# Kernel optimization log

Measured on AMD Instinct MI355X. Metric: run time of the kernel, lower is better.

Reference implementation:

```python
import jax, jax.numpy as jnp
import numpy as np

N = 16384      # nodes
E = 131072     # edges
D = 768        # in_size = hid_size = out_size (LayerNorm(768) hardcoded)
NT = 4         # num edge types (TypedLinear num_types)
NB = 3         # num bases (basis regularizer)
LN_EPS = 1e-5


def _layernorm(x, gamma, beta):
    mu = jnp.mean(x, axis=-1, keepdims=True)
    var = jnp.mean(jnp.square(x - mu), axis=-1, keepdims=True)
    return (x - mu) * jax.lax.rsqrt(var + LN_EPS) * gamma + beta


def setup_inputs() -> dict:
    key = jax.random.key(0)
    ks = jax.random.split(key, 16)
    s = 0.02  # weight init scale
    return {
        "h": jax.random.normal(ks[0], (N, D), jnp.float32),
        # TypedLinear basis params: W = sum_b coeff[t,b] * basis[b]
        "W_text": jax.random.normal(ks[1], (NB, D, D), jnp.float32) * s,
        "coeff_text": jax.random.normal(ks[2], (NT, NB), jnp.float32),
        "W_user": jax.random.normal(ks[3], (NB, D, D), jnp.float32) * s,
        "coeff_user": jax.random.normal(ks[4], (NT, NB), jnp.float32),
        "W_dst": jax.random.normal(ks[5], (NB, D, D), jnp.float32) * s,
        "coeff_dst": jax.random.normal(ks[6], (NT, NB), jnp.float32),
        "ln_gamma": jnp.ones((D,), jnp.float32),
        "ln_beta": jnp.zeros((D,), jnp.float32),
        "W_lin": jax.random.normal(ks[7], (2 * D, D), jnp.float32) * s,
        "b_lin": jnp.zeros((D,), jnp.float32),
        "src": jax.random.randint(ks[8], (E,), 0, N, dtype=jnp.int32),
        "dst": jax.random.randint(ks[9], (E,), 0, N, dtype=jnp.int32),
        "etype": jax.random.randint(ks[10], (E,), 0, NT, dtype=jnp.int32),
        "hete": jax.random.randint(ks[11], (E,), 0, 2, dtype=jnp.int32),
    }


def reference(h, W_text, coeff_text, W_user, coeff_user, W_dst, coeff_dst,
              ln_gamma, ln_beta, W_lin, b_lin, src, dst, etype, hete):
    # eval mode: dropout = identity
    x = _layernorm(h, ln_gamma, ln_beta)                       # [N, D]
    # Typed-linear via basis decomposition, folded per (type, node): [NT, N, D]
    Ht = jnp.einsum('nd,bdh,tb->tnh', x, W_text, coeff_text)
    Hu = jnp.einsum('nd,bdh,tb->tnh', x, W_user, coeff_user)
    Hd = jnp.einsum('nd,bdh,tb->tnh', x, W_dst, coeff_dst)

    mask = hete > 0                                            # hete vs homo edges
    # per-edge routed source message: [E, D]
    ef = jnp.where(mask[:, None],
                   jax.nn.relu(Ht[etype, src]),
                   jax.nn.relu(Hu[etype, src]))
    # Original concatenates [hete_feat, homo_feat] along edge dim, i.e. a stable
    # permutation putting hete edges first; dst features stay in original order.
    perm = jnp.argsort((~mask).astype(jnp.int32), stable=True)
    feat_perm = ef[perm]                                       # [E, D]
    dfeat = jax.nn.relu(Hd[etype, dst])                        # [E, D]
    m = jnp.concatenate([feat_perm, dfeat], axis=-1)           # [E, 2D]
    # scatter-sum messages to destination nodes
    n = jax.ops.segment_sum(m, dst, num_segments=N)            # [N, 2D]
    z = jax.nn.relu(n @ W_lin + b_lin)                         # [N, D]
    zn = jnp.linalg.norm(z, ord=2, axis=1, keepdims=True)
    zn = jnp.where(zn == 0, jnp.asarray(1.0, z.dtype), zn)
    return z / zn
```

## Files before the change

kernel.cpp:

```cpp
#include <hip/hip_runtime.h>
#include <hip/hip_bf16.h>
#include <cstdint>

static constexpr int N_  = 16384;
static constexpr int E_  = 131072;
static constexpr int D_  = 768;
static constexpr int D2_ = 1536;
static constexpr int DSQ_ = D_ * D_;

static constexpr size_t OFF_XB   = 0;
static constexpr size_t OFF_WCT  = 25165824;
static constexpr size_t OFF_WLT  = 39321600;
static constexpr size_t OFF_NB16 = 41680896;
static constexpr size_t OFF_H4   = 92012544;
static constexpr size_t OFF_ZB   = 92012544;
static constexpr size_t OFF_N1C  = 192675840;
static constexpr size_t OFF_TG   = 217841664;
static constexpr size_t OFF_PAY  = 218365952;
static constexpr size_t OFF_CNT  = 218890240;
static constexpr size_t OFF_BASE = 219152384;
static constexpr size_t OFF_CUR  = 219217936;
static constexpr size_t OFF_BC   = 219283472;
static constexpr size_t OFF_SCAN = 219285520;

typedef __attribute__((ext_vector_type(8))) short short8v;
typedef __attribute__((ext_vector_type(4))) float floatx4;

__device__ __forceinline__ void gld16(const void* g, void* l) {
  __builtin_amdgcn_global_load_lds(
      (const __attribute__((address_space(1))) unsigned int*)g,
      (__attribute__((address_space(3))) unsigned int*)l, 16, 0, 0);
}

__device__ __forceinline__ float b2f(short u) {
  union { unsigned int i; float f; } x;
  x.i = ((unsigned int)(unsigned short)u) << 16;
  return x.f;
}

__device__ __forceinline__ float wave_sum(float v) {
#pragma unroll
  for (int o = 32; o; o >>= 1) v += __shfl_down(v, o, 64);
  return v;
}

__global__ __launch_bounds__(256) void combine_wt_kernel(
    const float* __restrict__ Wt, const float* __restrict__ ct,
    const float* __restrict__ Wu, const float* __restrict__ cu,
    const float* __restrict__ Wd, const float* __restrict__ cd,
    __hip_bfloat16* __restrict__ WcT) {
  int i  = blockIdx.x * 256 + threadIdx.x;
  int ft = blockIdx.y;
  int f = ft >> 2, t = ft & 3;
  const float* W = (f == 0) ? Wt : ((f == 1) ? Wu : Wd);
  const float* c = ((f == 0) ? ct : ((f == 1) ? cu : cd)) + t * 3;
  float v = c[0] * W[i] + c[1] * W[DSQ_ + i] + c[2] * W[2 * DSQ_ + i];
  int d = i / D_, h = i % D_;
  WcT[(size_t)ft * DSQ_ + (size_t)h * D_ + d] = __float2bfloat16(v);
}

__global__ __launch_bounds__(256) void wlint_kernel(
    const float* __restrict__ W, __hip_bfloat16* __restrict__ WT) {
  int i = blockIdx.x * 256 + threadIdx.x;
  int k = i / D_, h = i % D_;
  WT[(size_t)h * D2_ + k] = __float2bfloat16(W[i]);
}

__global__ __launch_bounds__(256) void ln_kernel(
    const float* __restrict__ h, const float* __restrict__ gamma,
    const float* __restrict__ beta, __hip_bfloat16* __restrict__ x) {
  int v = blockIdx.x, tid = threadIdx.x;
  const float* hr = h + (size_t)v * D_;
  float e0 = hr[tid], e1 = hr[tid + 256], e2 = hr[tid + 512];
  float s = e0 + e1 + e2;
  float q = e0 * e0 + e1 * e1 + e2 * e2;
  __shared__ float red[8];
  __shared__ float mv[2];
  float ws_ = wave_sum(s), wq = wave_sum(q);
  int lane = tid & 63, w = tid >> 6;
  if (lane == 0) { red[w] = ws_; red[4 + w] = wq; }
  __syncthreads();
  if (tid == 0) {
    float S = red[0] + red[1] + red[2] + red[3];
    float Q = red[4] + red[5] + red[6] + red[7];
    float mu = S * (1.0f / D_);
    float var = Q * (1.0f / D_) - mu * mu;
    mv[0] = mu;
    mv[1] = rsqrtf(var + 1e-5f);
  }
  __syncthreads();
  float mu = mv[0], rstd = mv[1];
  __hip_bfloat16* xr = x + (size_t)v * D_;
  xr[tid]       = __float2bfloat16((e0 - mu) * rstd * gamma[tid]       + beta[tid]);
  xr[tid + 256] = __float2bfloat16((e1 - mu) * rstd * gamma[tid + 256] + beta[tid + 256]);
  xr[tid + 512] = __float2bfloat16((e2 - mu) * rstd * gamma[tid + 512] + beta[tid + 512]);
}

__global__ __launch_bounds__(256) void edge_a_kernel(
    const int* __restrict__ hete, const int* __restrict__ dst,
    const int* __restrict__ etype, int* __restrict__ blockcnt,
    int* __restrict__ cnt4) {
  int j = blockIdx.x * 256 + threadIdx.x;
  int flag = hete[j] > 0;
  unsigned long long m = __ballot(flag);
  __shared__ int wsum[4];
  int lane = threadIdx.x & 63, w = threadIdx.x >> 6;
  if (lane == 0) wsum[w] = __popcll(m);
  __syncthreads();
  if (threadIdx.x == 0)
    blockcnt[blockIdx.x] = wsum[0] + wsum[1] + wsum[2] + wsum[3];
  atomicAdd(&cnt4[dst[j] * 4 + etype[j]], 1);
}

__global__ __launch_bounds__(512) void scan_kernel(
    const int* __restrict__ blockcnt, int* __restrict__ scanout) {
  __shared__ int s[512];
  int t = threadIdx.x;
  int v = blockcnt[t];
  s[t] = v;
  __syncthreads();
  for (int o = 1; o < 512; o <<= 1) {
    int add = (t >= o) ? s[t - o] : 0;
    __syncthreads();
    s[t] += add;
    __syncthreads();
  }
  scanout[t] = s[t] - v;
  if (t == 511) scanout[512] = s[511];
}

__global__ __launch_bounds__(256) void edge_b_kernel(
    const int* __restrict__ hete, const int* __restrict__ dst,
    const int* __restrict__ scanout, int* __restrict__ target) {
  int j = blockIdx.x * 256 + threadIdx.x;
  int flag = hete[j] > 0;
  unsigned long long m = __ballot(flag);
  __shared__ int wsum[4];
  int lane = threadIdx.x & 63, w = threadIdx.x >> 6;
  if (lane == 0) wsum[w] = __popcll(m);
  __syncthreads();
  int wpre = 0;
#pragma unroll
  for (int i = 0; i < 4; i++) wpre += (i < w) ? wsum[i] : 0;
  int lpre = __popcll(m & ((1ull << lane) - 1ull));
  int hcum = scanout[blockIdx.x] + wpre + lpre;
  int K = scanout[512];
  int e = flag ? hcum : (K + j - hcum);
  target[j] = dst[e];
}

__global__ __launch_bounds__(1024) void base_scan_kernel(
    const int* __restrict__ cnt4, int* __restrict__ base) {
  __shared__ int s[1024];
  int t = threadIdx.x;
  int loc[16];
  int sum = 0;
#pragma unroll
  for (int i = 0; i < 16; i++) {
    int v = t * 16 + i;
    int d = cnt4[v * 4] + cnt4[v * 4 + 1] + cnt4[v * 4 + 2] + cnt4[v * 4 + 3];
    loc[i] = sum;
    sum += d;
  }
  s[t] = sum;
  __syncthreads();
  for (int o = 1; o < 1024; o <<= 1) {
    int add = (t >= o) ? s[t - o] : 0;
    __syncthreads();
    s[t] += add;
    __syncthreads();
  }
  int pre = t ? s[t - 1] : 0;
#pragma unroll
  for (int i = 0; i < 16; i++) base[t * 16 + i] = pre + loc[i];
  if (t == 1023) base[N_] = s[1023];
}

__global__ __launch_bounds__(256) void edge_sort_kernel(
    const int* __restrict__ target, const int* __restrict__ src,
    const int* __restrict__ etype, const int* __restrict__ hete,
    const int* __restrict__ base, int* __restrict__ cursor,
    int* __restrict__ payload) {
  int j = blockIdx.x * 256 + threadIdx.x;
  int v = target[j];
  int p = base[v] + atomicAdd(&cursor[v], 1);
  int g = ((hete[j] > 0) ? 0 : 4) + etype[j];
  payload[p] = (g << 14) | src[j];
}

template <bool FIRST>
__global__ __launch_bounds__(256) void gather_n1_kernel(
    const __hip_bfloat16* __restrict__ H, const int* __restrict__ base,
    const int* __restrict__ payload, __hip_bfloat16* __restrict__ n1c,
    __hip_bfloat16* __restrict__ nb16, int g0) {
  int wv = threadIdx.x >> 6, lane = threadIdx.x & 63;
  int v = blockIdx.x * 4 + wv;
  int b0 = base[v], b1 = base[v + 1];
  float acc[12];
  if (FIRST) {
#pragma unroll
    for (int i = 0; i < 12; i++) acc[i] = 0.f;
  } else {
    short8v a8 = *(const short8v*)(n1c + (size_t)v * D_ + lane * 8);
    short4  b4 = *(const short4*)(n1c + (size_t)v * D_ + 512 + lane * 4);
#pragma unroll
    for (int i = 0; i < 8; i++) acc[i] = b2f(a8[i]);
    acc[8] = b2f(b4.x); acc[9] = b2f(b4.y);
    acc[10] = b2f(b4.z); acc[11] = b2f(b4.w);
  }
  for (int idx = b0; idx < b1; ++idx) {
    int pl = payload[idx];
    int g = (pl >> 14) - g0;
    if ((unsigned)g > 3u) continue;
    const __hip_bfloat16* row = H + ((size_t)g * N_ + (pl & 16383)) * D_;
    short8v a8 = *(const short8v*)(row + lane * 8);
    short4  b4 = *(const short4*)(row + 512 + lane * 4);
#pragma unroll
    for (int i = 0; i < 8; i++) acc[i] += b2f(a8[i]);
    acc[8] += b2f(b4.x); acc[9] += b2f(b4.y);
    acc[10] += b2f(b4.z); acc[11] += b2f(b4.w);
  }
  __hip_bfloat16 o[12];
#pragma unroll
  for (int i = 0; i < 12; i++) o[i] = __float2bfloat16(acc[i]);
  if (FIRST) {
    *(short8v*)(n1c + (size_t)v * D_ + lane * 8) = *(const short8v*)o;
    *(short4*)(n1c + (size_t)v * D_ + 512 + lane * 4) = *(const short4*)(o + 8);
  } else {
    *(short8v*)(nb16 + (size_t)v * D2_ + lane * 8) = *(const short8v*)o;
    *(short4*)(nb16 + (size_t)v * D2_ + 512 + lane * 4) = *(const short4*)(o + 8);
  }
}

__global__ __launch_bounds__(256) void combine_n2_kernel(
    const __hip_bfloat16* __restrict__ H4, const int* __restrict__ cnt4,
    __hip_bfloat16* __restrict__ nb16) {
  size_t i = ((size_t)blockIdx.x * 256 + threadIdx.x) * 8;
  int v = (int)(i / D_);
  int k = (int)(i % D_);
  float acc[8] = {0.f, 0.f, 0.f, 0.f, 0.f, 0.f, 0.f, 0.f};
#pragma unroll
  for (int t = 0; t < 4; t++) {
    float c = (float)cnt4[v * 4 + t];
    if (c != 0.f) {
      short8v hv = *(const short8v*)(H4 + (size_t)t * N_ * D_ + i);
#pragma unroll
      for (int j = 0; j < 8; j++) acc[j] += c * b2f(hv[j]);
    }
  }
  __hip_bfloat16 o[8];
#pragma unroll
  for (int j = 0; j < 8; j++) o[j] = __float2bfloat16(acc[j]);
  *(short8v*)(nb16 + (size_t)v * D2_ + D_ + k) = *(const short8v*)o;
}

template <bool BIAS, bool OUTBF16>
__global__ __launch_bounds__(256) void gemm_mfma_kernel(
    const __hip_bfloat16* __restrict__ A, const __hip_bfloat16* __restrict__ BT0,
    const float* __restrict__ bias, void* __restrict__ Cv,
    int M, int N, int K, size_t strideB, size_t strideC) {
  const __hip_bfloat16* BT = BT0 + (size_t)blockIdx.z * strideB;
  __shared__ char lds[32768];
  char* As = lds;
  char* Bs = lds + 16384;
  int tid = threadIdx.x;
  int lane = tid & 63;
  int wv = tid >> 6;
  int wr = wv >> 1, wc = wv & 1;
  int nwg = gridDim.x * gridDim.y;
  int id = blockIdx.y * gridDim.x + blockIdx.x;
  int s = (id & 7) * (nwg >> 3) + (id >> 3);
  int bx = s % gridDim.x, by = s / gridDim.x;
  int row0 = by * 128, col0 = bx * 128;
  int r_ = tid >> 3;
  int s_ = tid & 7;

  floatx4 acc[4][4];
#pragma unroll
  for (int i = 0; i < 4; i++)
#pragma unroll
    for (int j = 0; j < 4; j++) acc[i][j] = floatx4{0.f, 0.f, 0.f, 0.f};

  for (int k0 = 0; k0 < K; k0 += 64) {
    __syncthreads();
#pragma unroll
    for (int is = 0; is < 4; is++) {
      int r = is * 32 + r_;
      int sp = s_ ^ (r & 7);
      gld16(A  + (size_t)(row0 + r) * K + k0 + sp * 8, As + is * 4096 + tid * 16);
      gld16(BT + (size_t)(col0 + r) * K + k0 + sp * 8, Bs + is * 4096 + tid * 16);
    }
    __syncthreads();
#pragma unroll
    for (int kk = 0; kk < 64; kk += 32) {
      int p = (kk >> 3) + (lane >> 4);
      short8v af[4], bf[4];
#pragma unroll
      for (int m = 0; m < 4; m++) {
        int ra = wr * 64 + m * 16 + (lane & 15);
        af[m] = *(const short8v*)(As + ra * 128 + ((p ^ (ra & 7)) << 4));
        int rb = wc * 64 + m * 16 + (lane & 15);
        bf[m] = *(const short8v*)(Bs + rb * 128 + ((p ^ (rb & 7)) << 4));
      }
#pragma unroll
      for (int m = 0; m < 4; m++)
#pragma unroll
        for (int n = 0; n < 4; n++)
          acc[m][n] = __builtin_amdgcn_mfma_f32_16x16x32_bf16(
              af[m], bf[n], acc[m][n], 0, 0, 0);
    }
  }
#pragma unroll
  for (int m = 0; m < 4; m++) {
#pragma unroll
    for (int n = 0; n < 4; n++) {
      int col = col0 + wc * 64 + n * 16 + (lane & 15);
      float bv = BIAS ? bias[col] : 0.f;
#pragma unroll
      for (int q = 0; q < 4; q++) {
        int row = row0 + wr * 64 + m * 16 + (lane >> 4) * 4 + q;
        float v = fmaxf(acc[m][n][q] + bv, 0.f);
        if constexpr (OUTBF16) {
          ((__hip_bfloat16*)Cv + (size_t)blockIdx.z * strideC)
              [(size_t)row * N + col] = __float2bfloat16(v);
        } else {
          ((float*)Cv + (size_t)blockIdx.z * strideC)
              [(size_t)row * N + col] = v;
        }
      }
    }
  }
}

__global__ __launch_bounds__(256) void norm_kernel(
    const float* __restrict__ z, float* __restrict__ out) {
  int v = blockIdx.x, tid = threadIdx.x;
  const float* zr = z + (size_t)v * D_;
  float e0 = zr[tid], e1 = zr[tid + 256], e2 = zr[tid + 512];
  float q = e0 * e0 + e1 * e1 + e2 * e2;
  __shared__ float red[4];
  __shared__ float sc;
  float wq = wave_sum(q);
  int lane = tid & 63, w = tid >> 6;
  if (lane == 0) red[w] = wq;
  __syncthreads();
  if (tid == 0) {
    float S = red[0] + red[1] + red[2] + red[3];
    float norm = sqrtf(S);
    sc = (norm == 0.f) ? 1.f : (1.f / norm);
  }
  __syncthreads();
  float s = sc;
  float* orow = out + (size_t)v * D_;
  orow[tid]       = e0 * s;
  orow[tid + 256] = e1 * s;
  orow[tid + 512] = e2 * s;
}

extern "C" void kernel_launch(void* const* d_in, const int* in_sizes, int n_in,
                              void* d_out, int out_size, void* d_ws,
                              size_t ws_size, hipStream_t stream) {
  (void)in_sizes; (void)n_in; (void)out_size; (void)ws_size;
  const float* h      = (const float*)d_in[0];
  const float* W_text = (const float*)d_in[1];
  const float* c_text = (const float*)d_in[2];
  const float* W_user = (const float*)d_in[3];
  const float* c_user = (const float*)d_in[4];
  const float* W_dst  = (const float*)d_in[5];
  const float* c_dst  = (const float*)d_in[6];
  const float* gamma  = (const float*)d_in[7];
  const float* beta   = (const float*)d_in[8];
  const float* W_lin  = (const float*)d_in[9];
  const float* b_lin  = (const float*)d_in[10];
  const int* src      = (const int*)d_in[11];
  const int* dst      = (const int*)d_in[12];
  const int* etype    = (const int*)d_in[13];
  const int* hete     = (const int*)d_in[14];
  float* out          = (float*)d_out;

  char* ws = (char*)d_ws;
  __hip_bfloat16* xb   = (__hip_bfloat16*)(ws + OFF_XB);
  __hip_bfloat16* WcT  = (__hip_bfloat16*)(ws + OFF_WCT);
  __hip_bfloat16* WlT  = (__hip_bfloat16*)(ws + OFF_WLT);
  __hip_bfloat16* nb16 = (__hip_bfloat16*)(ws + OFF_NB16);
  __hip_bfloat16* H4   = (__hip_bfloat16*)(ws + OFF_H4);
  float* zbuf          = (float*)(ws + OFF_ZB);
  __hip_bfloat16* n1c  = (__hip_bfloat16*)(ws + OFF_N1C);
  int* target   = (int*)(ws + OFF_TG);
  int* payload  = (int*)(ws + OFF_PAY);
  int* cnt4     = (int*)(ws + OFF_CNT);
  int* base     = (int*)(ws + OFF_BASE);
  int* cursor   = (int*)(ws + OFF_CUR);
  int* blockcnt = (int*)(ws + OFF_BC);
  int* scanout  = (int*)(ws + OFF_SCAN);

  hipMemsetAsync(cnt4, 0, (size_t)N_ * 4 * 4, stream);
  hipMemsetAsync(cursor, 0, (size_t)N_ * 4, stream);

  combine_wt_kernel<<<dim3(DSQ_ / 256, 12), 256, 0, stream>>>(
      W_text, c_text, W_user, c_user, W_dst, c_dst, WcT);
  wlint_kernel<<<(D2_ * D_) / 256, 256, 0, stream>>>(W_lin, WlT);
  ln_kernel<<<N_, 256, 0, stream>>>(h, gamma, beta, xb);
  edge_a_kernel<<<E_ / 256, 256, 0, stream>>>(hete, dst, etype, blockcnt, cnt4);
  scan_kernel<<<1, 512, 0, stream>>>(blockcnt, scanout);
  edge_b_kernel<<<E_ / 256, 256, 0, stream>>>(hete, dst, scanout, target);
  base_scan_kernel<<<1, 1024, 0, stream>>>(cnt4, base);
  edge_sort_kernel<<<E_ / 256, 256, 0, stream>>>(target, src, etype, hete,
                                                 base, cursor, payload);

  const size_t HSTRIDE = (size_t)N_ * D_;

  gemm_mfma_kernel<false, true>
      <<<dim3(D_ / 128, N_ / 128, 4), 256, 0, stream>>>(
          xb, WcT + (size_t)8 * DSQ_, nullptr, H4, N_, D_, D_, DSQ_, HSTRIDE);
  combine_n2_kernel<<<(N_ * D_) / (256 * 8), 256, 0, stream>>>(H4, cnt4, nb16);

  gemm_mfma_kernel<false, true>
      <<<dim3(D_ / 128, N_ / 128, 4), 256, 0, stream>>>(
          xb, WcT, nullptr, H4, N_, D_, D_, DSQ_, HSTRIDE);
  gather_n1_kernel<true><<<N_ / 4, 256, 0, stream>>>(H4, base, payload, n1c,
                                                     nb16, 0);
  gemm_mfma_kernel<false, true>
      <<<dim3(D_ / 128, N_ / 128, 4), 256, 0, stream>>>(
          xb, WcT + (size_t)4 * DSQ_, nullptr, H4, N_, D_, D_, DSQ_, HSTRIDE);
  gather_n1_kernel<false><<<N_ / 4, 256, 0, stream>>>(H4, base, payload, n1c,
                                                      nb16, 4);

  gemm_mfma_kernel<true, false>
      <<<dim3(D_ / 128, N_ / 128, 1), 256, 0, stream>>>(
          nb16, WlT, b_lin, zbuf, N_, D_, D2_, 0, 0);
  norm_kernel<<<N_, 256, 0, stream>>>(zbuf, out);
}
```

Baseline: 509.6 us.

## Replace GEMM with 256x128 tile, 512 threads, triple-buffered LDS pipeline

The bf16 MFMA GEMM is rewritten to use 256x128 output tiles with 8 waves and a three-stage LDS ring buffer. Global loads for k+2 are issued while MFMAs run on stage k, with explicit vmcnt/lgkmcnt waits, raised wave priority around the MFMAs, and two barrier phases per k-step. The intent is to hide global-load latency and raise reuse of the B tile. It uses 144KB of LDS per workgroup, which limits occupancy to one block per CU and halves the grid size.

```diff
diff --git a/kernel.cpp b/kernel.cpp
--- a/kernel.cpp
+++ b/kernel.cpp
@@ -254,26 +254,35 @@
   *(short8v*)(nb16 + (size_t)v * D2_ + D_ + k) = *(const short8v*)o;
 }
 
+__device__ __forceinline__ void stage_unit(const __hip_bfloat16* src, int K,
+                                           int row_base, int k0,
+                                           char* ldsbase, int tid) {
+#pragma unroll
+  for (int j = 0; j < 2; j++) {
+    int r = j * 64 + (tid >> 3);
+    int sp = (tid & 7) ^ (r & 7);
+    gld16(src + (size_t)(row_base + r) * K + k0 + sp * 8,
+          ldsbase + j * 8192 + tid * 16);
+  }
+}
+
 template <bool BIAS, bool OUTBF16>
-__global__ __launch_bounds__(256) void gemm_mfma_kernel(
+__global__ __launch_bounds__(512) void gemm256_kernel(
     const __hip_bfloat16* __restrict__ A, const __hip_bfloat16* __restrict__ BT0,
     const float* __restrict__ bias, void* __restrict__ Cv,
     int M, int N, int K, size_t strideB, size_t strideC) {
   const __hip_bfloat16* BT = BT0 + (size_t)blockIdx.z * strideB;
-  __shared__ char lds[32768];
-  char* As = lds;
-  char* Bs = lds + 16384;
-  int tid = threadIdx.x;
-  int lane = tid & 63;
-  int wv = tid >> 6;
-  int wr = wv >> 1, wc = wv & 1;
+  __shared__ char lds[147456];
+  const int tid = threadIdx.x;
+  const int lane = tid & 63;
+  const int wv = tid >> 6;
+  const int wr = wv >> 1, wc = wv & 1;
   int nwg = gridDim.x * gridDim.y;
   int id = blockIdx.y * gridDim.x + blockIdx.x;
-  int s = (id & 7) * (nwg >> 3) + (id >> 3);
-  int bx = s % gridDim.x, by = s / gridDim.x;
-  int row0 = by * 128, col0 = bx * 128;
-  int r_ = tid >> 3;
-  int s_ = tid & 7;
+  int sz = (id & 7) * (nwg >> 3) + (id >> 3);
+  int bx = sz % gridDim.x, by = sz / gridDim.x;
+  int row0 = by * 256, col0 = bx * 128;
+  const int nt = K >> 6;
 
   floatx4 acc[4][4];
 #pragma unroll
@@ -281,45 +290,80 @@
 #pragma unroll
     for (int j = 0; j < 4; j++) acc[i][j] = floatx4{0.f, 0.f, 0.f, 0.f};
 
-  for (int k0 = 0; k0 < K; k0 += 64) {
-    __syncthreads();
-#pragma unroll
-    for (int is = 0; is < 4; is++) {
-      int r = is * 32 + r_;
-      int sp = s_ ^ (r & 7);
-      gld16(A  + (size_t)(row0 + r) * K + k0 + sp * 8, As + is * 4096 + tid * 16);
-      gld16(BT + (size_t)(col0 + r) * K + k0 + sp * 8, Bs + is * 4096 + tid * 16);
-    }
-    __syncthreads();
-#pragma unroll
-    for (int kk = 0; kk < 64; kk += 32) {
-      int p = (kk >> 3) + (lane >> 4);
-      short8v af[4], bf[4];
+#pragma unroll
+  for (int kk = 0; kk < 2; kk++) {
+    char* nb = lds + kk * 49152;
+    stage_unit(A, K, row0, kk * 64, nb, tid);
+    stage_unit(A, K, row0 + 128, kk * 64, nb + 16384, tid);
+    stage_unit(BT, K, col0, kk * 64, nb + 32768, tid);
+  }
+  asm volatile("s_waitcnt vmcnt(6)" ::: "memory");
+  __builtin_amdgcn_s_barrier();
+  asm volatile("" ::: "memory");
+
+  for (int k = 0; k < nt; k++) {
+    char* buf = lds + (k % 3) * 49152;
+#pragma unroll
+    for (int ph = 0; ph < 2; ph++) {
+      short8v af[4][2], bf[2][2];
 #pragma unroll
       for (int m = 0; m < 4; m++) {
         int ra = wr * 64 + m * 16 + (lane & 15);
-        af[m] = *(const short8v*)(As + ra * 128 + ((p ^ (ra & 7)) << 4));
-        int rb = wc * 64 + m * 16 + (lane & 15);
-        bf[m] = *(const short8v*)(Bs + rb * 128 + ((p ^ (rb & 7)) << 4));
+#pragma unroll
+        for (int ks = 0; ks < 2; ks++) {
+          int p = ks * 4 + (lane >> 4);
+          af[m][ks] = *(const short8v*)(buf + ra * 128 + ((p ^ (ra & 7)) << 4));
+        }
       }
 #pragma unroll
+      for (int n = 0; n < 2; n++) {
+        int cb = wc * 64 + ph * 32 + n * 16 + (lane & 15);
+#pragma unroll
+        for (int ks = 0; ks < 2; ks++) {
+          int p = ks * 4 + (lane >> 4);
+          bf[n][ks] = *(const short8v*)(buf + 32768 + cb * 128 +
+                                        ((p ^ (cb & 7)) << 4));
+        }
+      }
+      if (k + 2 < nt) {
+        char* nb = lds + ((k + 2) % 3) * 49152;
+        if (ph == 0) {
+          stage_unit(A, K, row0, (k + 2) * 64, nb, tid);
+          stage_unit(A, K, row0 + 128, (k + 2) * 64, nb + 16384, tid);
+        } else {
+          stage_unit(BT, K, col0, (k + 2) * 64, nb + 32768, tid);
+        }
+      }
+      __builtin_amdgcn_s_barrier();
+      asm volatile("s_waitcnt lgkmcnt(0)" ::: "memory");
+      __builtin_amdgcn_s_setprio(1);
+#pragma unroll
       for (int m = 0; m < 4; m++)
 #pragma unroll
-        for (int n = 0; n < 4; n++)
-          acc[m][n] = __builtin_amdgcn_mfma_f32_16x16x32_bf16(
-              af[m], bf[n], acc[m][n], 0, 0, 0);
+        for (int n = 0; n < 2; n++)
+#pragma unroll
+          for (int ks = 0; ks < 2; ks++)
+            acc[m][ph * 2 + n] = __builtin_amdgcn_mfma_f32_16x16x32_bf16(
+                af[m][ks], bf[n][ks], acc[m][ph * 2 + n], 0, 0, 0);
+      __builtin_amdgcn_s_setprio(0);
+      if (ph == 1 && k + 1 < nt) {
+        if (k + 2 < nt) asm volatile("s_waitcnt vmcnt(6)" ::: "memory");
+        else            asm volatile("s_waitcnt vmcnt(0)" ::: "memory");
+      }
+      __builtin_amdgcn_s_barrier();
+      asm volatile("" ::: "memory");
     }
   }
 #pragma unroll
   for (int m = 0; m < 4; m++) {
 #pragma unroll
-    for (int n = 0; n < 4; n++) {
-      int col = col0 + wc * 64 + n * 16 + (lane & 15);
+    for (int j = 0; j < 4; j++) {
+      int col = col0 + wc * 64 + (j >> 1) * 32 + (j & 1) * 16 + (lane & 15);
       float bv = BIAS ? bias[col] : 0.f;
 #pragma unroll
       for (int q = 0; q < 4; q++) {
         int row = row0 + wr * 64 + m * 16 + (lane >> 4) * 4 + q;
-        float v = fmaxf(acc[m][n][q] + bv, 0.f);
+        float v = fmaxf(acc[m][j][q] + bv, 0.f);
         if constexpr (OUTBF16) {
           ((__hip_bfloat16*)Cv + (size_t)blockIdx.z * strideC)
               [(size_t)row * N + col] = __float2bfloat16(v);
@@ -409,25 +453,22 @@
                                                  base, cursor, payload);
 
   const size_t HSTRIDE = (size_t)N_ * D_;
-
-  gemm_mfma_kernel<false, true>
-      <<<dim3(D_ / 128, N_ / 128, 4), 256, 0, stream>>>(
-          xb, WcT + (size_t)8 * DSQ_, nullptr, H4, N_, D_, D_, DSQ_, HSTRIDE);
+  const dim3 ggrid(D_ / 128, N_ / 256, 4);
+
+  gemm256_kernel<false, true><<<ggrid, 512, 0, stream>>>(
+      xb, WcT + (size_t)8 * DSQ_, nullptr, H4, N_, D_, D_, DSQ_, HSTRIDE);
   combine_n2_kernel<<<(N_ * D_) / (256 * 8), 256, 0, stream>>>(H4, cnt4, nb16);
 
-  gemm_mfma_kernel<false, true>
-      <<<dim3(D_ / 128, N_ / 128, 4), 256, 0, stream>>>(
-          xb, WcT, nullptr, H4, N_, D_, D_, DSQ_, HSTRIDE);
+  gemm256_kernel<false, true><<<ggrid, 512, 0, stream>>>(
+      xb, WcT, nullptr, H4, N_, D_, D_, DSQ_, HSTRIDE);
   gather_n1_kernel<true><<<N_ / 4, 256, 0, stream>>>(H4, base, payload, n1c,
                                                      nb16, 0);
-  gemm_mfma_kernel<false, true>
-      <<<dim3(D_ / 128, N_ / 128, 4), 256, 0, stream>>>(
-          xb, WcT + (size_t)4 * DSQ_, nullptr, H4, N_, D_, D_, DSQ_, HSTRIDE);
+  gemm256_kernel<false, true><<<ggrid, 512, 0, stream>>>(
+      xb, WcT + (size_t)4 * DSQ_, nullptr, H4, N_, D_, D_, DSQ_, HSTRIDE);
   gather_n1_kernel<false><<<N_ / 4, 256, 0, stream>>>(H4, base, payload, n1c,
                                                       nb16, 4);
 
-  gemm_mfma_kernel<true, false>
-      <<<dim3(D_ / 128, N_ / 128, 1), 256, 0, stream>>>(
-          nb16, WlT, b_lin, zbuf, N_, D_, D2_, 0, 0);
+  gemm256_kernel<true, false><<<dim3(D_ / 128, N_ / 256, 1), 512, 0, stream>>>(
+      nb16, WlT, b_lin, zbuf, N_, D_, D2_, 0, 0);
   norm_kernel<<<N_, 256, 0, stream>>>(zbuf, out);
 }
```

New measurement: 558.6 us. +9.6%, slower.

## Replace GEMM with 256x256-tile, 8-wave, double-buffered pipelined MFMA kernel

Applied to the files above, without the earlier changes.

Replaces the 128x128 single-buffered GEMM with a 256x256 tile kernel using 512 threads and 128KB of LDS. Loads for the next K tile are issued during MFMA compute on the current one, with ping-pong buffers, explicit vmcnt waits, barriers and s_setprio. The LDS swizzle is reorganised and blockIdx.z is folded into the tile-grouping remap. The larger tile cuts global-memory traffic per FLOP and hides load latency. In exchange it runs one workgroup per CU, and grid counts drop to 768 blocks for the typed GEMMs and 192 for the final one, which may leave CUs idle.

```diff
diff --git a/kernel.cpp b/kernel.cpp
--- a/kernel.cpp
+++ b/kernel.cpp
@@ -254,78 +254,136 @@
   *(short8v*)(nb16 + (size_t)v * D2_ + D_ + k) = *(const short8v*)o;
 }
 
+__device__ __forceinline__ int fragaddr(int r, int p) {
+  int u = r >> 1;
+  int s = ((r & 1) << 2) | p;
+  return u * 128 + ((s ^ (u & 7)) << 4);
+}
+
+__device__ __forceinline__ void stage_kh(const __hip_bfloat16* X, int K,
+                                         int rowbase, int kglob, char* unit,
+                                         int tid) {
+#pragma unroll
+  for (int j = 0; j < 2; j++) {
+    int q = j * 512 + tid;
+    int u = q >> 3;
+    int sp = q & 7;
+    int s = sp ^ (u & 7);
+    int r = (u << 1) | (s >> 2);
+    int p = s & 3;
+    gld16(X + (size_t)(rowbase + r) * K + kglob + p * 8, unit + q * 16);
+  }
+}
+
 template <bool BIAS, bool OUTBF16>
-__global__ __launch_bounds__(256) void gemm_mfma_kernel(
+__global__ __launch_bounds__(512, 1) void gemm8p_kernel(
     const __hip_bfloat16* __restrict__ A, const __hip_bfloat16* __restrict__ BT0,
     const float* __restrict__ bias, void* __restrict__ Cv,
     int M, int N, int K, size_t strideB, size_t strideC) {
-  const __hip_bfloat16* BT = BT0 + (size_t)blockIdx.z * strideB;
-  __shared__ char lds[32768];
-  char* As = lds;
-  char* Bs = lds + 16384;
-  int tid = threadIdx.x;
-  int lane = tid & 63;
-  int wv = tid >> 6;
-  int wr = wv >> 1, wc = wv & 1;
-  int nwg = gridDim.x * gridDim.y;
-  int id = blockIdx.y * gridDim.x + blockIdx.x;
+  __shared__ char lds[131072];
+  const int tid = threadIdx.x, lane = tid & 63, wv = tid >> 6;
+  const int wr = wv >> 2, wcn = wv & 3;
+  int gx = gridDim.x, gz = gridDim.z;
+  int nwg = gx * gridDim.y * gz;
+  int id = (blockIdx.z * gridDim.y + blockIdx.y) * gx + blockIdx.x;
   int s = (id & 7) * (nwg >> 3) + (id >> 3);
-  int bx = s % gridDim.x, by = s / gridDim.x;
-  int row0 = by * 128, col0 = bx * 128;
-  int r_ = tid >> 3;
-  int s_ = tid & 7;
-
-  floatx4 acc[4][4];
-#pragma unroll
-  for (int i = 0; i < 4; i++)
+  int bx = s % gx;
+  int rem = s / gx;
+  int z = rem % gz;
+  int by = rem / gz;
+  const __hip_bfloat16* BT = BT0 + (size_t)z * strideB;
+  int row0 = by * 256, col0 = bx * 256;
+  const int nt = K >> 6, ni = nt >> 1;
+
+  floatx4 acc[8][4];
+#pragma unroll
+  for (int i = 0; i < 8; i++)
 #pragma unroll
     for (int j = 0; j < 4; j++) acc[i][j] = floatx4{0.f, 0.f, 0.f, 0.f};
 
-  for (int k0 = 0; k0 < K; k0 += 64) {
-    __syncthreads();
-#pragma unroll
-    for (int is = 0; is < 4; is++) {
-      int r = is * 32 + r_;
-      int sp = s_ ^ (r & 7);
-      gld16(A  + (size_t)(row0 + r) * K + k0 + sp * 8, As + is * 4096 + tid * 16);
-      gld16(BT + (size_t)(col0 + r) * K + k0 + sp * 8, Bs + is * 4096 + tid * 16);
+  stage_kh(A, K, row0, 0, lds, tid);
+  stage_kh(BT, K, col0, 0, lds + 32768, tid);
+  stage_kh(A, K, row0, 32, lds + 16384, tid);
+  stage_kh(BT, K, col0, 32, lds + 49152, tid);
+  asm volatile("s_waitcnt vmcnt(4)" ::: "memory");
+  __builtin_amdgcn_s_barrier();
+  asm volatile("" ::: "memory");
+
+  for (int it = 0; it < ni; ++it) {
+#pragma unroll
+    for (int half = 0; half < 2; ++half) {
+      char* rbuf = lds + (half << 16);
+      char* sbuf = lds + ((half ^ 1) << 16);
+      int stile = 2 * it + 1 + half;
+      bool do_stage = stile < nt;
+      int kg0 = stile * 64;
+      short8v af[8];
+#pragma unroll
+      for (int ks = 0; ks < 2; ++ks) {
+#pragma unroll
+        for (int ch = 0; ch < 2; ++ch) {
+          char* Au = rbuf + ks * 16384;
+          char* Bu = rbuf + 32768 + ks * 16384;
+          if (ch == 0) {
+#pragma unroll
+            for (int rf = 0; rf < 8; ++rf) {
+              int r = wr * 128 + rf * 16 + (lane & 15);
+              af[rf] = *(const short8v*)(Au + fragaddr(r, lane >> 4));
+            }
+          }
+          short8v bfr[2];
+#pragma unroll
+          for (int nf = 0; nf < 2; ++nf) {
+            int r = wcn * 64 + ch * 32 + nf * 16 + (lane & 15);
+            bfr[nf] = *(const short8v*)(Bu + fragaddr(r, lane >> 4));
+          }
+          if (do_stage) {
+            if (ch == 0)
+              stage_kh(A, K, row0, kg0 + ks * 32, sbuf + ks * 16384, tid);
+            else
+              stage_kh(BT, K, col0, kg0 + ks * 32, sbuf + 32768 + ks * 16384,
+                       tid);
+          }
+          asm volatile("" ::: "memory");
+          __builtin_amdgcn_s_barrier();
+          asm volatile("" ::: "memory");
+          __builtin_amdgcn_s_setprio(1);
+#pragma unroll
+          for (int rf = 0; rf < 8; ++rf)
+#pragma unroll
+            for (int nf = 0; nf < 2; ++nf)
+              acc[rf][ch * 2 + nf] = __builtin_amdgcn_mfma_f32_16x16x32_bf16(
+                  af[rf], bfr[nf], acc[rf][ch * 2 + nf], 0, 0, 0);
+          __builtin_amdgcn_s_setprio(0);
+          if (ch == 1) {
+            if (it == ni - 1 && half == 1) {
+              if (ks == 0) asm volatile("s_waitcnt vmcnt(0)" ::: "memory");
+            } else {
+              asm volatile("s_waitcnt vmcnt(4)" ::: "memory");
+            }
+          }
+          asm volatile("" ::: "memory");
+          __builtin_amdgcn_s_barrier();
+          asm volatile("" ::: "memory");
+        }
+      }
     }
-    __syncthreads();
-#pragma unroll
-    for (int kk = 0; kk < 64; kk += 32) {
-      int p = (kk >> 3) + (lane >> 4);
-      short8v af[4], bf[4];
-#pragma unroll
-      for (int m = 0; m < 4; m++) {
-        int ra = wr * 64 + m * 16 + (lane & 15);
-        af[m] = *(const short8v*)(As + ra * 128 + ((p ^ (ra & 7)) << 4));
-        int rb = wc * 64 + m * 16 + (lane & 15);
-        bf[m] = *(const short8v*)(Bs + rb * 128 + ((p ^ (rb & 7)) << 4));
-      }
-#pragma unroll
-      for (int m = 0; m < 4; m++)
-#pragma unroll
-        for (int n = 0; n < 4; n++)
-          acc[m][n] = __builtin_amdgcn_mfma_f32_16x16x32_bf16(
-              af[m], bf[n], acc[m][n], 0, 0, 0);
-    }
-  }
-#pragma unroll
-  for (int m = 0; m < 4; m++) {
-#pragma unroll
-    for (int n = 0; n < 4; n++) {
-      int col = col0 + wc * 64 + n * 16 + (lane & 15);
+  }
+#pragma unroll
+  for (int rf = 0; rf < 8; ++rf) {
+#pragma unroll
+    for (int j = 0; j < 4; ++j) {
+      int col = col0 + wcn * 64 + (j >> 1) * 32 + (j & 1) * 16 + (lane & 15);
       float bv = BIAS ? bias[col] : 0.f;
 #pragma unroll
-      for (int q = 0; q < 4; q++) {
-        int row = row0 + wr * 64 + m * 16 + (lane >> 4) * 4 + q;
-        float v = fmaxf(acc[m][n][q] + bv, 0.f);
+      for (int q = 0; q < 4; ++q) {
+        int row = row0 + wr * 128 + rf * 16 + (lane >> 4) * 4 + q;
+        float v = fmaxf(acc[rf][j][q] + bv, 0.f);
         if constexpr (OUTBF16) {
-          ((__hip_bfloat16*)Cv + (size_t)blockIdx.z * strideC)
-              [(size_t)row * N + col] = __float2bfloat16(v);
+          ((__hip_bfloat16*)Cv + (size_t)z * strideC)[(size_t)row * N + col] =
+              __float2bfloat16(v);
         } else {
-          ((float*)Cv + (size_t)blockIdx.z * strideC)
-              [(size_t)row * N + col] = v;
+          ((float*)Cv + (size_t)z * strideC)[(size_t)row * N + col] = v;
         }
       }
     }
@@ -409,25 +467,22 @@
                                                  base, cursor, payload);
 
   const size_t HSTRIDE = (size_t)N_ * D_;
-
-  gemm_mfma_kernel<false, true>
-      <<<dim3(D_ / 128, N_ / 128, 4), 256, 0, stream>>>(
-          xb, WcT + (size_t)8 * DSQ_, nullptr, H4, N_, D_, D_, DSQ_, HSTRIDE);
+  const dim3 ggrid(D_ / 256, N_ / 256, 4);
+
+  gemm8p_kernel<false, true><<<ggrid, 512, 0, stream>>>(
+      xb, WcT + (size_t)8 * DSQ_, nullptr, H4, N_, D_, D_, DSQ_, HSTRIDE);
   combine_n2_kernel<<<(N_ * D_) / (256 * 8), 256, 0, stream>>>(H4, cnt4, nb16);
 
-  gemm_mfma_kernel<false, true>
-      <<<dim3(D_ / 128, N_ / 128, 4), 256, 0, stream>>>(
-          xb, WcT, nullptr, H4, N_, D_, D_, DSQ_, HSTRIDE);
+  gemm8p_kernel<false, true><<<ggrid, 512, 0, stream>>>(
+      xb, WcT, nullptr, H4, N_, D_, D_, DSQ_, HSTRIDE);
   gather_n1_kernel<true><<<N_ / 4, 256, 0, stream>>>(H4, base, payload, n1c,
                                                      nb16, 0);
-  gemm_mfma_kernel<false, true>
-      <<<dim3(D_ / 128, N_ / 128, 4), 256, 0, stream>>>(
-          xb, WcT + (size_t)4 * DSQ_, nullptr, H4, N_, D_, D_, DSQ_, HSTRIDE);
+  gemm8p_kernel<false, true><<<ggrid, 512, 0, stream>>>(
+      xb, WcT + (size_t)4 * DSQ_, nullptr, H4, N_, D_, D_, DSQ_, HSTRIDE);
   gather_n1_kernel<false><<<N_ / 4, 256, 0, stream>>>(H4, base, payload, n1c,
                                                       nb16, 4);
 
-  gemm_mfma_kernel<true, false>
-      <<<dim3(D_ / 128, N_ / 128, 1), 256, 0, stream>>>(
-          nb16, WlT, b_lin, zbuf, N_, D_, D2_, 0, 0);
+  gemm8p_kernel<true, false><<<dim3(D_ / 256, N_ / 256, 1), 512, 0, stream>>>(
+      nb16, WlT, b_lin, zbuf, N_, D_, D2_, 0, 0);
   norm_kernel<<<N_, 256, 0, stream>>>(zbuf, out);
 }
```

After: 494.7 us. 1.03x faster.
